# Kernel optimization log

Hardware: AMD Instinct MI355X
Metric: run time of the kernel (lower is better)

## Reference

```python
import jax, jax.numpy as jnp
import numpy as np

B, N, C, Q, H, RATIO = 8, 8700, 256, 300, 8, 4
D = C // H
HID = C * RATIO
EPS = 1e-5


def _ln(x, w, b):
    m = jnp.mean(x, axis=-1, keepdims=True)
    v = jnp.mean((x - m) ** 2, axis=-1, keepdims=True)
    return (x - m) * jax.lax.rsqrt(v + EPS) * w + b


def setup_inputs() -> dict:
    key = jax.random.key(0)
    ks = jax.random.split(key, 8)
    s = 0.02
    return {
        "x": jax.random.normal(ks[0], (B, N, C), jnp.float32),
        # linear weights stored [in, out] (y = x @ W), no biases (qkv_bias=False, Mlp bias=False)
        "Wq": jax.random.normal(ks[1], (C, C), jnp.float32) * s,
        "Wk": jax.random.normal(ks[2], (C, C), jnp.float32) * s,
        "Wv": jax.random.normal(ks[3], (C, C), jnp.float32) * s,
        "Wp": jax.random.normal(ks[4], (C, C), jnp.float32) * s,
        "W1": jax.random.normal(ks[5], (C, HID), jnp.float32) * s,
        "W2": jax.random.normal(ks[6], (HID, C), jnp.float32) * s,
        "ln1_w": jnp.ones((C,), jnp.float32),
        "ln1_b": jnp.zeros((C,), jnp.float32),
        "ln2_w": jnp.ones((C,), jnp.float32),
        "ln2_b": jnp.zeros((C,), jnp.float32),
        "gamma1": jnp.ones((C,), jnp.float32),
        "gamma2": jnp.ones((C,), jnp.float32),
    }


def reference(x, Wq, Wk, Wv, Wp, W1, W2, ln1_w, ln1_b, ln2_w, ln2_b, gamma1, gamma2):
    scale = D ** -0.5
    xn = _ln(x, ln1_w, ln1_b)                       # [B,N,C]
    # SAQAttn: queries only from the first Q tokens; keys/values from all N tokens
    q = (xn[:, :Q] @ Wq).reshape(B, Q, H, D) * scale  # [B,Q,H,D]
    k = (xn @ Wk).reshape(B, N, H, D)
    v = (xn @ Wv).reshape(B, N, H, D)
    attn = jax.nn.softmax(jnp.einsum('bqhd,bnhd->bhqn', q, k), axis=-1)  # [B,H,Q,N]
    x_det = jnp.einsum('bhqn,bnhd->bqhd', attn, v).reshape(B, Q, C) @ Wp  # [B,Q,C]
    # residual with layer-scale gamma1; context tokens pass normed features through
    x_attn = jnp.concatenate([x_det, xn[:, Q:]], axis=1)
    x = x + gamma1 * x_attn
    # tokens_norm=False: norm2 only on query tokens
    x = jnp.concatenate([_ln(x[:, :Q], ln2_w, ln2_b), x[:, Q:]], axis=1)
    # MLP on query tokens with layer-scale gamma2 (exact GELU, as nn.GELU default)
    det = gamma2 * (jax.nn.gelu(x[:, :Q] @ W1, approximate=False) @ W2)
    # faithful to source: x_res + cat([det, x[:,Q:]]) doubles the context tokens
    return x + jnp.concatenate([det, x[:, Q:]], axis=1)
```

## Files before the change

### kernel.cpp

```cpp
#include <hip/hip_runtime.h>

#define BB 8
#define NN 8700
#define CC 256
#define QQ 300
#define HH 8
#define DD 32
#define HIDN 1024
#define NSPLIT 16
#define TSTR (NSPLIT * 64)
#define KSLACK 1536

typedef unsigned short u16;
typedef __attribute__((ext_vector_type(8))) short short8;
typedef __attribute__((ext_vector_type(4))) float f32x4;

#define MFMA16(a, b, c) __builtin_amdgcn_mfma_f32_16x16x32_bf16((a), (b), (c), 0, 0, 0)

__device__ __forceinline__ u16 f2bu(float f) {
    unsigned int u = __builtin_bit_cast(unsigned int, f);
    u += 0x7fffu + ((u >> 16) & 1u);
    return (u16)(u >> 16);
}
__device__ __forceinline__ unsigned int cvtpk(float lo, float hi) {
    unsigned int r;
    asm("v_cvt_pk_bf16_f32 %0, %1, %2" : "=v"(r) : "v"(lo), "v"(hi));
    return r;
}

__global__ __launch_bounds__(256)
void wprep_all(const float* __restrict__ Wq, const float* __restrict__ Wk,
               const float* __restrict__ Wv, const float* __restrict__ Wp,
               const float* __restrict__ W1, const float* __restrict__ W2,
               u16* __restrict__ dst, float qscale)
{
    int e = blockIdx.x * 256 + threadIdx.x;
    float v;
    if (e < 65536)       { int i = e;          int n = i >> 8, k = i & 255;   v = Wq[k * 256 + n] * qscale; }
    else if (e < 131072) { int i = e - 65536;  int n = i >> 8, k = i & 255;   v = Wk[k * 256 + n]; }
    else if (e < 196608) { int i = e - 131072; int n = i >> 8, k = i & 255;   v = Wv[k * 256 + n]; }
    else if (e < 262144) { int i = e - 196608; int n = i >> 8, k = i & 255;   v = Wp[k * 256 + n]; }
    else if (e < 524288) { int i = e - 262144; int n = i >> 8, k = i & 255;   v = W1[k * 1024 + n]; }
    else                 { int i = e - 524288; int n = i >> 10, k = i & 1023; v = W2[k * 256 + n]; }
    dst[e] = f2bu(v);
}

__global__ __launch_bounds__(256)
void ln1_k(const float* __restrict__ x, const float* __restrict__ w,
           const float* __restrict__ bv, const float* __restrict__ g1,
           u16* __restrict__ xn, float* __restrict__ out)
{
    int row = blockIdx.x * 4 + (threadIdx.x >> 6);
    int l = threadIdx.x & 63;
    size_t base = (size_t)row * CC + l * 4;
    float4 xv = *reinterpret_cast<const float4*>(x + base);
    float s  = xv.x + xv.y + xv.z + xv.w;
    float s2 = xv.x * xv.x + xv.y * xv.y + xv.z * xv.z + xv.w * xv.w;
#pragma unroll
    for (int m = 1; m < 64; m <<= 1) {
        s  += __shfl_xor(s,  m, 64);
        s2 += __shfl_xor(s2, m, 64);
    }
    float mean = s * (1.0f / CC);
    float rs = rsqrtf(s2 * (1.0f / CC) - mean * mean + 1e-5f);
    float4 wv = *reinterpret_cast<const float4*>(w  + l * 4);
    float4 bb = *reinterpret_cast<const float4*>(bv + l * 4);
    float n0 = (xv.x - mean) * rs * wv.x + bb.x;
    float n1 = (xv.y - mean) * rs * wv.y + bb.y;
    float n2 = (xv.z - mean) * rs * wv.z + bb.z;
    float n3 = (xv.w - mean) * rs * wv.w + bb.w;
    ushort4 u; u.x = f2bu(n0); u.y = f2bu(n1); u.z = f2bu(n2); u.w = f2bu(n3);
    *reinterpret_cast<ushort4*>(xn + base) = u;
    int n = row % NN;
    if (n >= QQ) {
        float4 gv = *reinterpret_cast<const float4*>(g1 + l * 4);
        float4 o;
        o.x = 2.0f * (xv.x + gv.x * n0);
        o.y = 2.0f * (xv.y + gv.y * n1);
        o.z = 2.0f * (xv.z + gv.z * n2);
        o.w = 2.0f * (xv.w + gv.w * n3);
        *reinterpret_cast<float4*>(out + base) = o;
    }
}

__global__ __launch_bounds__(256)
void ln2_k(const float* __restrict__ x, const float* __restrict__ pd,
           const float* __restrict__ g1, const float* __restrict__ w,
           const float* __restrict__ bv, float* __restrict__ xqf, u16* __restrict__ xqb)
{
    int r = blockIdx.x * 4 + (threadIdx.x >> 6);
    int l = threadIdx.x & 63;
    int b = r / QQ, n = r - b * QQ;
    size_t xoff = ((size_t)b * NN + n) * CC + l * 4;
    size_t roff = (size_t)r * CC + l * 4;
    float4 xv = *reinterpret_cast<const float4*>(x + xoff);
    float4 pv = *reinterpret_cast<const float4*>(pd + roff);
    float4 gv = *reinterpret_cast<const float4*>(g1 + l * 4);
    float x0 = xv.x + gv.x * pv.x;
    float x1 = xv.y + gv.y * pv.y;
    float x2 = xv.z + gv.z * pv.z;
    float x3 = xv.w + gv.w * pv.w;
    float s  = x0 + x1 + x2 + x3;
    float s2 = x0 * x0 + x1 * x1 + x2 * x2 + x3 * x3;
#pragma unroll
    for (int m = 1; m < 64; m <<= 1) {
        s  += __shfl_xor(s,  m, 64);
        s2 += __shfl_xor(s2, m, 64);
    }
    float mean = s * (1.0f / CC);
    float rs = rsqrtf(s2 * (1.0f / CC) - mean * mean + 1e-5f);
    float4 wv = *reinterpret_cast<const float4*>(w  + l * 4);
    float4 bb = *reinterpret_cast<const float4*>(bv + l * 4);
    float n0 = (x0 - mean) * rs * wv.x + bb.x;
    float n1 = (x1 - mean) * rs * wv.y + bb.y;
    float n2 = (x2 - mean) * rs * wv.z + bb.z;
    float n3 = (x3 - mean) * rs * wv.w + bb.w;
    float4 o; o.x = n0; o.y = n1; o.z = n2; o.w = n3;
    *reinterpret_cast<float4*>(xqf + roff) = o;
    ushort4 u; u.x = f2bu(n0); u.y = f2bu(n1); u.z = f2bu(n2); u.w = f2bu(n3);
    *reinterpret_cast<ushort4*>(xqb + roff) = u;
}

__global__ __launch_bounds__(512)
void gemm_kv(const u16* __restrict__ A, const u16* __restrict__ WT,
             u16* __restrict__ Cb, u16* __restrict__ Cb2, int M)
{
    __shared__ u16 alds[64 * 256];
    const int tid = threadIdx.x;
    const int w = tid >> 6, l = tid & 63;
    const int l15 = l & 15, kg = l >> 4;
    const int rowbase = blockIdx.x * 64;
    const f32x4 fz = {0.f, 0.f, 0.f, 0.f};

    {
        const char* gb = (const char*)(A + (size_t)rowbase * CC);
        char* lb = (char*)alds;
#pragma unroll
        for (int j = 0; j < 4; j++) {
            int o = tid * 64 + j * 16;
            short8 v = *reinterpret_cast<const short8*>(gb + o);
            int d = o ^ (((o >> 9) & 7) << 4);
            *reinterpret_cast<short8*>(lb + d) = v;
        }
    }
    __syncthreads();

    const int colbase = w * 64;
    const u16* bp[4];
#pragma unroll
    for (int ni = 0; ni < 4; ni++)
        bp[ni] = WT + (size_t)(colbase + ni * 16 + l15) * CC + kg * 8;

    f32x4 acc[4][4];
#pragma unroll
    for (int mi = 0; mi < 4; mi++)
#pragma unroll
        for (int ni = 0; ni < 4; ni++) acc[mi][ni] = fz;

    const char* lb = (const char*)alds;
    const int sw = (l15 & 7) << 4;
    int abase[4];
#pragma unroll
    for (int mi = 0; mi < 4; mi++) abase[mi] = (mi * 16 + l15) << 9;

#pragma unroll
    for (int ks = 0; ks < 8; ks++) {
        const int koff = ((ks * 64) + (kg * 16)) ^ sw;
        short8 a[4], bfr[4];
#pragma unroll
        for (int mi = 0; mi < 4; mi++)
            a[mi] = *reinterpret_cast<const short8*>(lb + abase[mi] + koff);
#pragma unroll
        for (int ni = 0; ni < 4; ni++)
            bfr[ni] = *reinterpret_cast<const short8*>(bp[ni] + ks * 32);
#pragma unroll
        for (int mi = 0; mi < 4; mi++)
#pragma unroll
            for (int ni = 0; ni < 4; ni++)
                acc[mi][ni] = MFMA16(a[mi], bfr[ni], acc[mi][ni]);
    }

#pragma unroll
    for (int mi = 0; mi < 4; mi++) {
#pragma unroll
        for (int j = 0; j < 4; j++) {
            int r = rowbase + mi * 16 + kg * 4 + j;
            if (r >= M) continue;
#pragma unroll
            for (int ni = 0; ni < 4; ni++) {
                int col = colbase + ni * 16 + l15;
                float v = acc[mi][ni][j];
                if (col < CC) Cb[(size_t)r * CC + col] = f2bu(v);
                else          Cb2[(size_t)r * CC + (col - CC)] = f2bu(v);
            }
        }
    }
}

template<int EPI, int MT>
__global__ __launch_bounds__(256)
void gemm_k(const u16* __restrict__ A, const u16* __restrict__ WT,
            u16* __restrict__ Cb, u16* __restrict__ Cb2, float* __restrict__ Cf,
            const float* __restrict__ basep, const float* __restrict__ gvec,
            float* __restrict__ outp,
            int M, int K, int ldC, int rpb, int bstr)
{
    constexpr int NM = MT / 16;
    const int w = threadIdx.x >> 6, l = threadIdx.x & 63;
    const int l15 = l & 15, kg = l >> 4;
    const int rowbase = blockIdx.x * MT;
    const int colbase = blockIdx.y * 256 + w * 64;
    const short8 z8 = {0, 0, 0, 0, 0, 0, 0, 0};
    const f32x4 fz = {0.f, 0.f, 0.f, 0.f};

    const u16* ap[NM]; bool av[NM];
#pragma unroll
    for (int mi = 0; mi < NM; mi++) {
        int r = rowbase + mi * 16 + l15;
        av[mi] = (r < M);
        int rr = av[mi] ? r : 0;
        size_t ar = (size_t)(rr / rpb) * bstr + (rr % rpb);
        ap[mi] = A + ar * K + kg * 8;
    }
    const u16* bp[4];
#pragma unroll
    for (int ni = 0; ni < 4; ni++) {
        int col = colbase + ni * 16 + l15;
        bp[ni] = WT + (size_t)col * K + kg * 8;
    }
    f32x4 acc[NM][4];
#pragma unroll
    for (int mi = 0; mi < NM; mi++)
#pragma unroll
        for (int ni = 0; ni < 4; ni++) acc[mi][ni] = fz;

    for (int ks = 0; ks < K; ks += 32) {
        short8 a[NM], bfr[4];
#pragma unroll
        for (int mi = 0; mi < NM; mi++)
            a[mi] = av[mi] ? *reinterpret_cast<const short8*>(ap[mi] + ks) : z8;
#pragma unroll
        for (int ni = 0; ni < 4; ni++)
            bfr[ni] = *reinterpret_cast<const short8*>(bp[ni] + ks);
#pragma unroll
        for (int mi = 0; mi < NM; mi++)
#pragma unroll
            for (int ni = 0; ni < 4; ni++)
                acc[mi][ni] = MFMA16(a[mi], bfr[ni], acc[mi][ni]);
    }
#pragma unroll
    for (int mi = 0; mi < NM; mi++) {
#pragma unroll
        for (int j = 0; j < 4; j++) {
            int r = rowbase + mi * 16 + kg * 4 + j;
            if (r >= M) continue;
#pragma unroll
            for (int ni = 0; ni < 4; ni++) {
                int col = colbase + ni * 16 + l15;
                float v = acc[mi][ni][j];
                if (EPI == 0) {
                    if (col < CC) Cb[(size_t)r * ldC + col] = f2bu(v);
                    else          Cb2[(size_t)r * ldC + (col - CC)] = f2bu(v);
                } else if (EPI == 1) {
                    float gl = 0.5f * v * (1.0f + erff(v * 0.70710678118654752f));
                    Cb[(size_t)r * ldC + col] = f2bu(gl);
                } else if (EPI == 2) {
                    Cf[(size_t)r * ldC + col] = v;
                } else {
                    float res = basep[(size_t)r * CC + col] + gvec[col] * v;
                    size_t orow = (size_t)(r / QQ) * NN + (r % QQ);
                    outp[orow * CC + col] = res;
                }
            }
        }
    }
}

__global__ __launch_bounds__(256)
void attn_k(const u16* __restrict__ qm, const u16* __restrict__ km,
            const u16* __restrict__ vm, float* __restrict__ Op,
            float* __restrict__ lp)
{
    __shared__ u16 vt[2][32 * 64];
    __shared__ u16 plds[4][2][16 * 64];

    const int bx = blockIdx.x;
    const int split = bx >> 6;
    const int rem = bx & 63;
    const int h = rem >> 3, b = rem & 7;
    const int bh = b * HH + h;
    const int tid = threadIdx.x;
    const int w = tid >> 6, l = tid & 63;
    const int l15 = l & 15, kg = l >> 4;
    const int tstart = split * 64;
    const int nt = (NN - tstart + TSTR - 1) / TSTR;

    const f32x4 fz = {0.f, 0.f, 0.f, 0.f};
    const short os = (short)0x3F80;
    const short8 ones = {os, os, os, os, os, os, os, os};

    const u16* kbase = km + (size_t)b * NN * CC + h * DD;
    const u16* vbase = vm + (size_t)b * NN * CC + h * DD;
    const int vkp = (tid & 31) * 2;
    const int vdg = (tid >> 5) * 4;

    short8 qfr[5];
#pragma unroll
    for (int qf = 0; qf < 5; qf++) {
        int qrow = w * 80 + qf * 16 + l15;
        int qc = qrow < QQ ? qrow : 0;
        qfr[qf] = *reinterpret_cast<const short8*>(qm + ((size_t)(b * QQ + qc) * CC + h * DD + kg * 8));
    }

    f32x4 o[2][5]; float lpart[5];
#pragma unroll
    for (int qf = 0; qf < 5; qf++) { o[0][qf] = fz; o[1][qf] = fz; lpart[qf] = 0.f; }

    short8 kf[4]; ushort4 v0r, v1r;
#pragma unroll
    for (int kb = 0; kb < 4; kb++)
        kf[kb] = *reinterpret_cast<const short8*>(kbase + (size_t)(tstart + kb * 16 + l15) * CC + kg * 8);
    v0r = *reinterpret_cast<const ushort4*>(vbase + (size_t)(tstart + vkp) * CC + vdg);
    v1r = *reinterpret_cast<const ushort4*>(vbase + (size_t)(tstart + vkp + 1) * CC + vdg);

    char* pl = (char*)plds[w];
    const int rdswz = ((l15 << 7) ^ ((l15 & 7) << 4)) + (kg << 4);
    const int wrbase = (l15 << 7) ^ ((l15 & 7) << 4);

    for (int t = 0; t < nt; ++t) {
        const int n0 = tstart + t * TSTR;
        char* vtb = (char*)vt[t & 1];
#pragma unroll
        for (int i = 0; i < 4; i++) {
            int row = vdg + i;
            unsigned int pk2 = (unsigned int)v0r[i] | ((unsigned int)v1r[i] << 16);
            int byteo = ((row << 7) + (vkp << 1)) ^ ((row & 7) << 4);
            *reinterpret_cast<unsigned int*>(vtb + byteo) = pk2;
        }
        __syncthreads();

        short8 kfn[4]; ushort4 v0n, v1n;
        { const int n0n = n0 + TSTR;
#pragma unroll
          for (int kb = 0; kb < 4; kb++)
              kfn[kb] = *reinterpret_cast<const short8*>(kbase + (size_t)(n0n + kb * 16 + l15) * CC + kg * 8);
          v0n = *reinterpret_cast<const ushort4*>(vbase + (size_t)(n0n + vkp) * CC + vdg);
          v1n = *reinterpret_cast<const ushort4*>(vbase + (size_t)(n0n + vkp + 1) * CC + vdg); }

        short8 va[2][2];
#pragma unroll
        for (int ks = 0; ks < 2; ks++)
#pragma unroll
            for (int dg = 0; dg < 2; dg++) {
                int row = dg * 16 + l15;
                int byteo = ((row << 7) + 64 * ks + 16 * kg) ^ ((row & 7) << 4);
                va[ks][dg] = *reinterpret_cast<const short8*>(vtb + byteo);
            }

        const bool tail = (n0 + 64 > NN);

#pragma unroll
        for (int qf = 0; qf < 5; qf++) {
            short8 bp0, bp1;
            if (qf > 0) {
                const char* plr = pl + (((qf - 1) & 1) << 11);
                bp0 = *reinterpret_cast<const short8*>(plr + rdswz);
                bp1 = *reinterpret_cast<const short8*>(plr + rdswz + 64);
            }
            f32x4 s[4];
            __builtin_amdgcn_s_setprio(1);
#pragma unroll
            for (int kb = 0; kb < 4; kb++)
                s[kb] = MFMA16(kf[kb], qfr[qf], fz);
            __builtin_amdgcn_s_setprio(0);
            char* plw = pl + ((qf & 1) << 11);
#pragma unroll
            for (int kb = 0; kb < 4; kb++) {
                float p0 = exp2f(s[kb][0]);
                float p1 = exp2f(s[kb][1]);
                float p2 = exp2f(s[kb][2]);
                float p3 = exp2f(s[kb][3]);
                if (tail) {
                    int kbase2 = n0 + 16 * kb + 4 * kg;
                    if (kbase2 + 0 >= NN) p0 = 0.f;
                    if (kbase2 + 1 >= NN) p1 = 0.f;
                    if (kbase2 + 2 >= NN) p2 = 0.f;
                    if (kbase2 + 3 >= NN) p3 = 0.f;
                }
                int byte0 = wrbase + ((16 * kb + 4 * kg) << 1);
                *reinterpret_cast<unsigned int*>(plw + byte0)     = cvtpk(p0, p1);
                *reinterpret_cast<unsigned int*>(plw + byte0 + 4) = cvtpk(p2, p3);
            }
            if (qf > 0) {
                __builtin_amdgcn_s_setprio(1);
                o[0][qf - 1] = MFMA16(va[0][0], bp0, o[0][qf - 1]);
                o[1][qf - 1] = MFMA16(va[0][1], bp0, o[1][qf - 1]);
                o[0][qf - 1] = MFMA16(va[1][0], bp1, o[0][qf - 1]);
                o[1][qf - 1] = MFMA16(va[1][1], bp1, o[1][qf - 1]);
                f32x4 tsum = MFMA16(ones, bp0, fz);
                tsum = MFMA16(ones, bp1, tsum);
                __builtin_amdgcn_s_setprio(0);
                lpart[qf - 1] += tsum[0];
            }
        }
        {
            const char* plr = pl + 0;
            short8 bp0 = *reinterpret_cast<const short8*>(plr + rdswz);
            short8 bp1 = *reinterpret_cast<const short8*>(plr + rdswz + 64);
            __builtin_amdgcn_s_setprio(1);
            o[0][4] = MFMA16(va[0][0], bp0, o[0][4]);
            o[1][4] = MFMA16(va[0][1], bp0, o[1][4]);
            o[0][4] = MFMA16(va[1][0], bp1, o[0][4]);
            o[1][4] = MFMA16(va[1][1], bp1, o[1][4]);
            f32x4 tsum = MFMA16(ones, bp0, fz);
            tsum = MFMA16(ones, bp1, tsum);
            __builtin_amdgcn_s_setprio(0);
            lpart[4] += tsum[0];
        }
#pragma unroll
        for (int kb = 0; kb < 4; kb++) kf[kb] = kfn[kb];
        v0r = v0n; v1r = v1n;
    }

    size_t pb = (size_t)(split * 64 + bh) * QQ;
#pragma unroll
    for (int qf = 0; qf < 5; qf++) {
        int q = w * 80 + qf * 16 + l15;
        if (q >= QQ) continue;
        size_t pr = pb + q;
        if (kg == 0) lp[pr] = lpart[qf];
        *reinterpret_cast<f32x4*>(Op + pr * DD + kg * 4)      = o[0][qf];
        *reinterpret_cast<f32x4*>(Op + pr * DD + 16 + kg * 4) = o[1][qf];
    }
}

__global__ __launch_bounds__(256)
void comb_k(const float* __restrict__ Op, const float* __restrict__ lp, u16* __restrict__ ao)
{
    int g = blockIdx.x * 256 + threadIdx.x;
    int d4 = (g & 7) * 4;
    int row = g >> 3;
    int bh = row / QQ, qq = row - bh * QQ;
    int b = bh >> 3, h = bh & 7;
    float L = 0.f, a0 = 0.f, a1 = 0.f, a2 = 0.f, a3 = 0.f;
#pragma unroll
    for (int s = 0; s < NSPLIT; s++) {
        size_t pr = (size_t)(s * 64 + bh) * QQ + qq;
        L += lp[pr];
        float4 ov = *reinterpret_cast<const float4*>(Op + pr * DD + d4);
        a0 += ov.x; a1 += ov.y; a2 += ov.z; a3 += ov.w;
    }
    float inv = 1.0f / L;
    ushort4 u;
    u.x = f2bu(a0 * inv); u.y = f2bu(a1 * inv); u.z = f2bu(a2 * inv); u.w = f2bu(a3 * inv);
    *reinterpret_cast<ushort4*>(ao + ((size_t)(b * QQ + qq) * CC + h * DD + d4)) = u;
}

extern "C" void kernel_launch(void* const* d_in, const int* in_sizes, int n_in,
                              void* d_out, int out_size, void* d_ws, size_t ws_size,
                              hipStream_t stream)
{
    (void)in_sizes; (void)n_in; (void)out_size; (void)ws_size;
    const float* x    = (const float*)d_in[0];
    const float* Wq   = (const float*)d_in[1];
    const float* Wk   = (const float*)d_in[2];
    const float* Wv   = (const float*)d_in[3];
    const float* Wp   = (const float*)d_in[4];
    const float* W1   = (const float*)d_in[5];
    const float* W2   = (const float*)d_in[6];
    const float* ln1w = (const float*)d_in[7];
    const float* ln1b = (const float*)d_in[8];
    const float* ln2w = (const float*)d_in[9];
    const float* ln2b = (const float*)d_in[10];
    const float* g1   = (const float*)d_in[11];
    const float* g2   = (const float*)d_in[12];
    float* out = (float*)d_out;

    char* p = (char*)d_ws;
    auto alloc = [&](size_t bytes) { char* r = p; p += (bytes + 255) & ~(size_t)255; return r; };

    const size_t MKV = (size_t)BB * NN;
    const size_t MQ  = (size_t)BB * QQ;

    u16* WqT  = (u16*)alloc((size_t)CC * CC * 2);
    u16* WkvT = (u16*)alloc((size_t)CC * CC * 2 * 2);
    u16* WpT  = (u16*)alloc((size_t)CC * CC * 2);
    u16* W1T  = (u16*)alloc((size_t)CC * HIDN * 2);
    u16* W2T  = (u16*)alloc((size_t)HIDN * CC * 2);
    u16* xn   = (u16*)alloc((MKV + 64) * CC * 2);
    u16* kbf  = (u16*)alloc((MKV + KSLACK) * CC * 2);
    u16* vbf  = (u16*)alloc((MKV + KSLACK) * CC * 2);
    u16* qbf  = (u16*)alloc(MQ * CC * 2);
    u16* aob  = (u16*)alloc(MQ * CC * 2);
    u16* xqb  = (u16*)alloc(MQ * CC * 2);
    u16* h1   = (u16*)alloc(MQ * HIDN * 2);
    float* pd  = (float*)alloc(MQ * CC * 4);
    float* xqf = (float*)alloc(MQ * CC * 4);
    float* Op  = (float*)alloc((size_t)NSPLIT * 64 * QQ * DD * 4);
    float* lp  = (float*)alloc((size_t)NSPLIT * 64 * QQ * 4);

    const float qscale = 0.17677669529663687f * 1.4426950408889634f;

    wprep_all<<<3072, 256, 0, stream>>>(Wq, Wk, Wv, Wp, W1, W2, WqT, qscale);

    ln1_k<<<(int)(MKV / 4), 256, 0, stream>>>(x, ln1w, ln1b, g1, xn, out);

    gemm_kv<<<1088, 512, 0, stream>>>(xn, WkvT, kbf, vbf, (int)MKV);
    gemm_k<0, 16><<<dim3(150, 1), 256, 0, stream>>>(xn, WqT, qbf, nullptr, nullptr, nullptr, nullptr, nullptr,
                                                    (int)MQ, CC, CC, QQ, NN);

    attn_k<<<64 * NSPLIT, 256, 0, stream>>>(qbf, kbf, vbf, Op, lp);
    comb_k<<<(int)(MQ * 8 / 256), 256, 0, stream>>>(Op, lp, aob);

    gemm_k<2, 16><<<dim3(150, 1), 256, 0, stream>>>(aob, WpT, nullptr, nullptr, pd, nullptr, nullptr, nullptr,
                                                    (int)MQ, CC, CC, (int)MQ, 0);
    ln2_k<<<(int)(MQ / 4), 256, 0, stream>>>(x, pd, g1, ln2w, ln2b, xqf, xqb);

    gemm_k<1, 16><<<dim3(150, 4), 256, 0, stream>>>(xqb, W1T, h1, nullptr, nullptr, nullptr, nullptr, nullptr,
                                                    (int)MQ, CC, HIDN, (int)MQ, 0);
    gemm_k<3, 16><<<dim3(150, 1), 256, 0, stream>>>(h1, W2T, nullptr, nullptr, nullptr, xqf, g2, out,
                                                    (int)MQ, HIDN, CC, (int)MQ, 0);
}
```

Baseline: 225.0 us.

## Stage attention K tiles via global_load_lds, raise split count, tile weight transpose

The attention kernel now loads each 64-row K tile directly into swizzled, double-buffered LDS with global_load_lds and reads the MFMA fragments from LDS, instead of prefetching them into registers. This is meant to cut register pressure and make the global loads more coalesced. The KV split count goes from 16 to 20 for more blocks and shorter per-block loops, at the cost of more partial results for the combine step to reduce. The weight-prep kernel is rewritten as an LDS-tiled transpose so both its reads and writes coalesce. Correctness depends on the async LDS loads having completed before the fragment reads, which relies on the existing barrier and wait behaviour.

```diff
diff --git a/kernel.cpp b/kernel.cpp
--- a/kernel.cpp
+++ b/kernel.cpp
@@ -7,7 +7,7 @@
 #define HH 8
 #define DD 32
 #define HIDN 1024
-#define NSPLIT 16
+#define NSPLIT 20
 #define TSTR (NSPLIT * 64)
 #define KSLACK 1536
 
@@ -27,22 +27,47 @@
     asm("v_cvt_pk_bf16_f32 %0, %1, %2" : "=v"(r) : "v"(lo), "v"(hi));
     return r;
 }
+__device__ __forceinline__ void gload16(const u16* g, u16* l) {
+    __builtin_amdgcn_global_load_lds(
+        (const __attribute__((address_space(1))) void*)g,
+        (__attribute__((address_space(3))) void*)l, 16, 0, 0);
+}
 
 __global__ __launch_bounds__(256)
-void wprep_all(const float* __restrict__ Wq, const float* __restrict__ Wk,
-               const float* __restrict__ Wv, const float* __restrict__ Wp,
-               const float* __restrict__ W1, const float* __restrict__ W2,
-               u16* __restrict__ dst, float qscale)
-{
-    int e = blockIdx.x * 256 + threadIdx.x;
-    float v;
-    if (e < 65536)       { int i = e;          int n = i >> 8, k = i & 255;   v = Wq[k * 256 + n] * qscale; }
-    else if (e < 131072) { int i = e - 65536;  int n = i >> 8, k = i & 255;   v = Wk[k * 256 + n]; }
-    else if (e < 196608) { int i = e - 131072; int n = i >> 8, k = i & 255;   v = Wv[k * 256 + n]; }
-    else if (e < 262144) { int i = e - 196608; int n = i >> 8, k = i & 255;   v = Wp[k * 256 + n]; }
-    else if (e < 524288) { int i = e - 262144; int n = i >> 8, k = i & 255;   v = W1[k * 1024 + n]; }
-    else                 { int i = e - 524288; int n = i >> 10, k = i & 1023; v = W2[k * 256 + n]; }
-    dst[e] = f2bu(v);
+void wprep_t(const float* __restrict__ Wq, const float* __restrict__ Wk,
+             const float* __restrict__ Wv, const float* __restrict__ Wp,
+             const float* __restrict__ W1, const float* __restrict__ W2,
+             u16* __restrict__ dst, float qscale)
+{
+    __shared__ u16 tl[64][66];
+    int bid = blockIdx.x;
+    const float* src; int K, N, tr, tc; size_t dof; float sc = 1.f;
+    if (bid < 64) {
+        int mat = bid >> 4, ti = bid & 15;
+        src = (mat == 0) ? Wq : (mat == 1) ? Wk : (mat == 2) ? Wv : Wp;
+        K = 256; N = 256; tr = ti >> 2; tc = ti & 3;
+        dof = (size_t)mat * 65536;
+        if (mat == 0) sc = qscale;
+    } else if (bid < 128) {
+        int ti = bid - 64; src = W1; K = 256; N = 1024; tr = ti >> 4; tc = ti & 15; dof = 262144;
+    } else {
+        int ti = bid - 128; src = W2; K = 1024; N = 256; tr = ti >> 2; tc = ti & 3; dof = 524288;
+    }
+    int tid = threadIdx.x;
+    int jj = tid & 63;
+    int i0 = tid >> 6;
+#pragma unroll
+    for (int ii = 0; ii < 16; ii++) {
+        int kk = i0 * 16 + ii;
+        float v = src[(size_t)(tr * 64 + kk) * N + tc * 64 + jj] * sc;
+        tl[kk][jj] = f2bu(v);
+    }
+    __syncthreads();
+#pragma unroll
+    for (int ii = 0; ii < 16; ii++) {
+        int nn = i0 * 16 + ii;
+        dst[dof + (size_t)(tc * 64 + nn) * K + tr * 64 + jj] = tl[jj][nn];
+    }
 }
 
 __global__ __launch_bounds__(256)
@@ -281,6 +306,7 @@
             const u16* __restrict__ vm, float* __restrict__ Op,
             float* __restrict__ lp)
 {
+    __shared__ u16 klds[2][64 * 32];
     __shared__ u16 vt[2][32 * 64];
     __shared__ u16 plds[4][2][16 * 64];
 
@@ -304,6 +330,10 @@
     const int vkp = (tid & 31) * 2;
     const int vdg = (tid >> 5) * 4;
 
+    const int krow  = (w << 4) + (l >> 2);
+    const int kslot = (l & 3) ^ ((krow >> 1) & 3);
+    const u16* ksrc = kbase + (size_t)krow * CC + kslot * 8;
+
     short8 qfr[5];
 #pragma unroll
     for (int qf = 0; qf < 5; qf++) {
@@ -316,12 +346,9 @@
 #pragma unroll
     for (int qf = 0; qf < 5; qf++) { o[0][qf] = fz; o[1][qf] = fz; lpart[qf] = 0.f; }
 
-    short8 kf[4]; ushort4 v0r, v1r;
-#pragma unroll
-    for (int kb = 0; kb < 4; kb++)
-        kf[kb] = *reinterpret_cast<const short8*>(kbase + (size_t)(tstart + kb * 16 + l15) * CC + kg * 8);
-    v0r = *reinterpret_cast<const ushort4*>(vbase + (size_t)(tstart + vkp) * CC + vdg);
-    v1r = *reinterpret_cast<const ushort4*>(vbase + (size_t)(tstart + vkp + 1) * CC + vdg);
+    gload16(ksrc + (size_t)tstart * CC, (u16*)((char*)klds[0] + (w << 10)));
+    ushort4 v0r = *reinterpret_cast<const ushort4*>(vbase + (size_t)(tstart + vkp) * CC + vdg);
+    ushort4 v1r = *reinterpret_cast<const ushort4*>(vbase + (size_t)(tstart + vkp + 1) * CC + vdg);
 
     char* pl = (char*)plds[w];
     const int rdswz = ((l15 << 7) ^ ((l15 & 7) << 4)) + (kg << 4);
@@ -339,13 +366,18 @@
         }
         __syncthreads();
 
-        short8 kfn[4]; ushort4 v0n, v1n;
-        { const int n0n = n0 + TSTR;
-#pragma unroll
-          for (int kb = 0; kb < 4; kb++)
-              kfn[kb] = *reinterpret_cast<const short8*>(kbase + (size_t)(n0n + kb * 16 + l15) * CC + kg * 8);
-          v0n = *reinterpret_cast<const ushort4*>(vbase + (size_t)(n0n + vkp) * CC + vdg);
-          v1n = *reinterpret_cast<const ushort4*>(vbase + (size_t)(n0n + vkp + 1) * CC + vdg); }
+        gload16(ksrc + (size_t)(n0 + TSTR) * CC, (u16*)((char*)klds[(t + 1) & 1] + (w << 10)));
+        ushort4 v0n = *reinterpret_cast<const ushort4*>(vbase + (size_t)(n0 + TSTR + vkp) * CC + vdg);
+        ushort4 v1n = *reinterpret_cast<const ushort4*>(vbase + (size_t)(n0 + TSTR + vkp + 1) * CC + vdg);
+
+        short8 kf[4];
+        { const char* klb = (const char*)klds[t & 1];
+#pragma unroll
+          for (int kb = 0; kb < 4; kb++) {
+              int row = kb * 16 + l15;
+              int off = (row << 6) + ((kg ^ ((row >> 1) & 3)) << 4);
+              kf[kb] = *reinterpret_cast<const short8*>(klb + off);
+          } }
 
         short8 va[2][2];
 #pragma unroll
@@ -417,8 +449,6 @@
             __builtin_amdgcn_s_setprio(0);
             lpart[4] += tsum[0];
         }
-#pragma unroll
-        for (int kb = 0; kb < 4; kb++) kf[kb] = kfn[kb];
         v0r = v0n; v1r = v1n;
     }
 
@@ -501,7 +531,7 @@
 
     const float qscale = 0.17677669529663687f * 1.4426950408889634f;
 
-    wprep_all<<<3072, 256, 0, stream>>>(Wq, Wk, Wv, Wp, W1, W2, WqT, qscale);
+    wprep_t<<<192, 256, 0, stream>>>(Wq, Wk, Wv, Wp, W1, W2, WqT, qscale);
 
     ln1_k<<<(int)(MKV / 4), 256, 0, stream>>>(x, ln1w, ln1b, g1, xn, out);
 
```

Result: no change. 228.1 us (+1.3%).
